# Performance work log

Measured on AMD Instinct MI355X. Metric: run time of the kernel, lower is better.

The kernel has to match this reference:

```python
import jax, jax.numpy as jnp
import numpy as np

B, L, K = 8, 512, 30
H, NUM_IN, NPTS = 128, 384, 8
EPS = 1e-8


def _linear_params(key, din, dout):
    kw, kb = jax.random.split(key)
    W = jax.random.normal(kw, (din, dout), jnp.float32) * 0.02
    b = jax.random.normal(kb, (dout,), jnp.float32) * 0.02
    return W, b


def setup_inputs() -> dict:
    key = jax.random.key(0)
    ks = jax.random.split(key, 10)
    h_V = jax.random.normal(ks[0], (B, L, H), jnp.float32)
    h_E = jax.random.normal(ks[1], (B, L, K, NUM_IN), jnp.float32)
    E_idx = jax.random.randint(ks[2], (B, L, K), 0, L)
    X_neighbors = jax.random.normal(ks[3], (B, L, K, 3, 3), jnp.float32) * 3.0
    mask_V = jnp.ones((B, L), jnp.float32)
    mask_attend = jnp.ones((B, L, K), jnp.float32)
    Wp, bp = _linear_params(ks[4], H, NPTS * 3)
    W1, b1 = _linear_params(ks[5], H + NUM_IN + 9 * NPTS, H)
    W2, b2 = _linear_params(ks[6], H, H)
    W3, b3 = _linear_params(ks[7], H, H)
    Wi, bi = _linear_params(ks[8], H, 4 * H)
    Wo, bo = _linear_params(ks[9], 4 * H, H)
    g1 = jnp.ones((H,), jnp.float32); be1 = jnp.zeros((H,), jnp.float32)
    g2 = jnp.ones((H,), jnp.float32); be2 = jnp.zeros((H,), jnp.float32)
    return dict(h_V=h_V, h_E=h_E, E_idx=E_idx, X_neighbors=X_neighbors,
                mask_V=mask_V, mask_attend=mask_attend,
                Wp=Wp, bp=bp, W1=W1, b1=b1, W2=W2, b2=b2, W3=W3, b3=b3,
                Wi=Wi, bi=bi, Wo=Wo, bo=bo, g1=g1, be1=be1, g2=g2, be2=be2)


def _frames(N, CA, C):
    # openfold Rigid.from_3_points (Gram-Schmidt): x-axis along CA-N, C in xy-plane
    e0 = CA - N
    e0 = e0 / jnp.sqrt(jnp.sum(e0 * e0, -1, keepdims=True) + EPS)
    e1 = C - CA
    e1 = e1 - e0 * jnp.sum(e0 * e1, -1, keepdims=True)
    e1 = e1 / jnp.sqrt(jnp.sum(e1 * e1, -1, keepdims=True) + EPS)
    e2 = jnp.cross(e0, e1)
    R = jnp.stack([e0, e1, e2], axis=-1)  # basis vectors as columns
    return R, CA


def _ln(x, g, b):
    m = jnp.mean(x, -1, keepdims=True)
    v = jnp.var(x, -1, keepdims=True)
    return (x - m) / jnp.sqrt(v + 1e-5) * g + b


def _forward(h_V, h_E, X_neighbors, mask_V, mask_attend, Wp, bp, W1, b1, W2, b2,
             W3, b3, Wi, bi, Wo, bo, g1, be1, g2, be2):
    gelu = lambda x: jax.nn.gelu(x, approximate=False)
    # per-neighbor backbone frames: [B,L,K,3,3], [B,L,K,3]
    R, t = _frames(X_neighbors[..., 0, :], X_neighbors[..., 1, :], X_neighbors[..., 2, :])
    h_V_prev = h_E[..., -H:]
    sh = h_E.shape[:-1]  # (B,L,K)
    p_ln = (h_V_prev @ Wp + bp).reshape(*sh, NPTS, 3)  # local points of each neighbor
    p_local = p_ln[:, :, 0]                            # [B,L,n,3] (self is neighbor 0)
    npg = jnp.einsum('blkij,blknj->blkni', R, p_ln) + t[..., None, :]  # global points
    p_global = npg[:, :, 0]
    pge = jnp.broadcast_to(p_global[:, :, None], npg.shape)
    ple = jnp.broadcast_to(p_local[:, :, None], npg.shape)
    pln = jnp.sqrt(jnp.sum(ple * ple, -1) + EPS)
    R0 = R[:, :, 0]; t0 = t[:, :, 0]  # self frame
    npl = jnp.einsum('blji,blknj->blkni', R0, npg - t0[:, :, None, None, :])  # invert_apply
    npl_norm = jnp.sqrt(jnp.sum(npl * npl, -1) + EPS)
    npg_norm = jnp.sqrt(jnp.sum((pge - npg) ** 2, -1) + EPS)
    node_expand = jnp.broadcast_to(h_V[:, :, None, :], (*sh, H))
    msg = jnp.concatenate([node_expand, h_E,
                           ple.reshape(*sh, -1), pln,
                           npl.reshape(*sh, -1), npl_norm, npg_norm], axis=-1)
    node_m = gelu(msg @ W1 + b1)
    node_m = gelu(node_m @ W2 + b2)
    node_m = node_m @ W3 + b3
    node_m = mask_attend[..., None] * node_m
    node_m = jnp.mean(node_m, axis=-2)
    h = _ln(h_V + node_m, g1, be1)  # dropout is identity in eval
    d = gelu(h @ Wi + bi) @ Wo + bo
    h = _ln(h + d, g2, be2)
    return mask_V[..., None] * h


def reference(h_V, h_E, E_idx, X_neighbors, mask_V, mask_attend, Wp, bp, W1, b1,
              W2, b2, W3, b3, Wi, bi, Wo, bo, g1, be1, g2, be2):
    # E_idx only defines the neighbor axis shape; geometry comes pre-gathered in X_neighbors/h_E
    return _forward(h_V, h_E, X_neighbors, mask_V, mask_attend, Wp, bp, W1, b1,
                    W2, b2, W3, b3, Wi, bi, Wo, bo, g1, be1, g2, be2)
```

## Files before the change

kernel.cpp:

```cpp
#include <hip/hip_runtime.h>

#define B_ 8
#define L_ 512
#define K_ 30
#define NIN_ 384
#define HES 11520
#define BUFW 136
#define GFW 96
#define PWU 4608
#define R0_OFF 0
#define T0_OFF 9
#define PL0_OFF 12
#define NPG_OFF 40
#define PLF_OFF 760
#define NM_OFF 640
#define GEOF_OFF 1520

#define W1F_OFF 0
#define W2F_OFF 77824
#define W3F_OFF 94208
#define WIF_OFF 110592
#define WOF_OFF 176128
#define WPF_OFF 241664

typedef __attribute__((ext_vector_type(8))) short short8;
typedef __attribute__((ext_vector_type(8))) unsigned short ushort8;
typedef __attribute__((ext_vector_type(4))) float floatx4;
typedef __attribute__((ext_vector_type(4))) float f32x4;

__device__ __forceinline__ float b2f(unsigned short u) {
    union { unsigned int i; float f; } x; x.i = ((unsigned int)u) << 16; return x.f;
}
__device__ __forceinline__ unsigned short f2b(float f) {
    unsigned int u = __builtin_bit_cast(unsigned int, f);
    return (unsigned short)((u + 0x7fffu + ((u >> 16) & 1u)) >> 16);
}
__device__ __forceinline__ float gelu_f(float x) {
    return 0.5f * x * (1.0f + erff(x * 0.70710678118654752440f));
}
__device__ __forceinline__ short8 pack8(const float* p) {
    f32x4 lo = *(const f32x4*)p;
    f32x4 hi = *(const f32x4*)(p + 4);
    short8 r;
    r[0] = (short)f2b(lo[0]); r[1] = (short)f2b(lo[1]);
    r[2] = (short)f2b(lo[2]); r[3] = (short)f2b(lo[3]);
    r[4] = (short)f2b(hi[0]); r[5] = (short)f2b(hi[1]);
    r[6] = (short)f2b(hi[2]); r[7] = (short)f2b(hi[3]);
    return r;
}
__device__ __forceinline__ float dot8(const float* hp, ushort8 v) {
    return hp[0] * b2f(v[0]) + hp[1] * b2f(v[1]) + hp[2] * b2f(v[2]) + hp[3] * b2f(v[3]) +
           hp[4] * b2f(v[4]) + hp[5] * b2f(v[5]) + hp[6] * b2f(v[6]) + hp[7] * b2f(v[7]);
}

__global__ __launch_bounds__(256) void prep_kernel(
        const float* __restrict__ W1, const float* __restrict__ W2,
        const float* __restrict__ W3, const float* __restrict__ Wi,
        const float* __restrict__ Wo, const float* __restrict__ Wp,
        unsigned short* __restrict__ ws) {
    int idx = blockIdx.x * 256 + threadIdx.x;
    if (idx < 94208 || (idx >= 241664 && idx < 245760)) {
        const float* in; int i, KC, Kreal, Nreal, Nld;
        if (idx < 77824)      { in = W1; i = idx;          KC = 19; Kreal = 584; Nreal = 128; Nld = 128; }
        else if (idx < 94208) { in = W2; i = idx - 77824;  KC = 4;  Kreal = 128; Nreal = 128; Nld = 128; }
        else                  { in = Wp; i = idx - 241664; KC = 4;  Kreal = 128; Nreal = 24;  Nld = 24;  }
        int f = i >> 9, r = i & 511;
        int ct = f / KC, kc = f % KC;
        int lane = r >> 3, j = r & 7;
        int q = lane >> 4, l = lane & 15;
        int k = kc * 32 + q * 8 + j, n = ct * 16 + l;
        ws[idx] = (k < Kreal && n < Nreal) ? f2b(in[k * Nld + n]) : (unsigned short)0;
    } else if (idx < 110592) {
        int i = idx - 94208;
        int f = i >> 9, r = i & 511;
        int ct = f >> 2, kc = f & 3;
        int lane = r >> 3, j = r & 7;
        int q = lane >> 4, l = lane & 15;
        ws[idx] = f2b(W3[(kc * 32 + q * 8 + j) * 128 + ct * 16 + l]);
    } else if (idx < 176128) {
        int i = idx - 110592;
        int c8 = i >> 12, r = i & 4095;
        int o = r >> 3, ii = r & 7;
        ws[idx] = f2b(Wi[(c8 * 8 + ii) * 512 + o]);
    } else if (idx < 241664) {
        int i = idx - 176128;
        int o8 = i >> 10, r = i & 1023;
        int c = r >> 3, ii = r & 7;
        ws[idx] = f2b(Wo[(o8 * 8 + ii) * 128 + c]);
    }
}

__global__ __launch_bounds__(128, 3) void main_kernel(
    const float* __restrict__ h_V,
    const float* __restrict__ h_E,
    const float* __restrict__ Xn,
    const float* __restrict__ mask_V,
    const float* __restrict__ mask_attend,
    const float* __restrict__ bp,
    const float* __restrict__ b1g,
    const float* __restrict__ b2g,
    const float* __restrict__ b3g,
    const float* __restrict__ big,
    const float* __restrict__ bog,
    const float* __restrict__ g1,
    const float* __restrict__ be1,
    const float* __restrict__ g2,
    const float* __restrict__ be2,
    const unsigned short* __restrict__ wsT,
    float* __restrict__ out) {

    __shared__ __align__(16) unsigned short lds[2 * PWU];

    const int tid  = threadIdx.x;
    const int wv   = tid >> 6;
    const int lane = tid & 63;
    const int quad = lane >> 4;
    const int l16  = lane & 15;
    const int ko   = quad * 8;
    const int site = blockIdx.x * 2 + wv;

    unsigned short* wl   = lds + wv * PWU;
    unsigned short* buf1 = wl;
    unsigned short* geoF = wl + GEOF_OFF;
    float*          Fv   = (float*)wl;

    const unsigned short* W1F = wsT + W1F_OFF;
    const unsigned short* W2F = wsT + W2F_OFF;
    const unsigned short* W3F = wsT + W3F_OFF;
    const unsigned short* WiF = wsT + WIF_OFF;
    const unsigned short* WoF = wsT + WOF_OFF;
    const unsigned short* WpF = wsT + WPF_OFF;

    const float* hEb = h_E + (size_t)site * HES;
    const float* hVb = h_V + site * 128;
    const short8 z8 = {0, 0, 0, 0, 0, 0, 0, 0};

    float maskR[2][4];
    for (int rt = 0; rt < 2; ++rt)
        for (int r = 0; r < 4; ++r) {
            int row = rt * 16 + quad * 4 + r;
            maskR[rt][r] = (row < K_) ? mask_attend[site * K_ + row] * (1.0f / 30.0f) : 0.0f;
        }

    float Rr[9], Tt[3];
    if (lane < K_) {
        const float* xp = Xn + ((size_t)site * K_ + lane) * 9;
        float Nx = xp[0], Ny = xp[1], Nz = xp[2];
        float Ax = xp[3], Ay = xp[4], Az = xp[5];
        float Cx = xp[6], Cy = xp[7], Cz = xp[8];
        float e0x = Ax - Nx, e0y = Ay - Ny, e0z = Az - Nz;
        float r0 = 1.0f / sqrtf(e0x * e0x + e0y * e0y + e0z * e0z + 1e-8f);
        e0x *= r0; e0y *= r0; e0z *= r0;
        float u1x = Cx - Ax, u1y = Cy - Ay, u1z = Cz - Az;
        float d = e0x * u1x + e0y * u1y + e0z * u1z;
        u1x -= e0x * d; u1y -= e0y * d; u1z -= e0z * d;
        float r1 = 1.0f / sqrtf(u1x * u1x + u1y * u1y + u1z * u1z + 1e-8f);
        u1x *= r1; u1y *= r1; u1z *= r1;
        Rr[0] = e0x; Rr[1] = u1x; Rr[2] = e0y * u1z - e0z * u1y;
        Rr[3] = e0y; Rr[4] = u1y; Rr[5] = e0z * u1x - e0x * u1z;
        Rr[6] = e0z; Rr[7] = u1z; Rr[8] = e0x * u1y - e0y * u1x;
        Tt[0] = Ax; Tt[1] = Ay; Tt[2] = Az;
    }

    {
        floatx4 a[2][2] = {{{0,0,0,0},{0,0,0,0}},{{0,0,0,0},{0,0,0,0}}};
        for (int kc = 0; kc < 4; ++kc) {
            int col = 256 + kc * 32 + ko;
            short8 fa0 = pack8(hEb + l16 * NIN_ + col);
            int r1 = 16 + l16;
            short8 fa1 = (r1 < K_) ? pack8(hEb + r1 * NIN_ + col) : z8;
            for (int ct = 0; ct < 2; ++ct) {
                short8 fb = *(const short8*)(WpF + (ct * 4 + kc) * 512 + lane * 8);
                a[0][ct] = __builtin_amdgcn_mfma_f32_16x16x32_bf16(fa0, fb, a[0][ct], 0, 0, 0);
                a[1][ct] = __builtin_amdgcn_mfma_f32_16x16x32_bf16(fa1, fb, a[1][ct], 0, 0, 0);
            }
        }
        for (int ct = 0; ct < 2; ++ct) {
            int ccol = ct * 16 + l16;
            if (ccol < 24) {
                float bpc = bp[ccol];
                for (int rt = 0; rt < 2; ++rt)
                    for (int i = 0; i < 4; ++i) {
                        int row = rt * 16 + quad * 4 + i;
                        if (row < K_) Fv[PLF_OFF + row * 24 + ccol] = a[rt][ct][i] + bpc;
                    }
            }
        }
    }

    if (lane < K_) {
        float pl[24];
        #pragma unroll
        for (int c = 0; c < 24; ++c) pl[c] = Fv[PLF_OFF + lane * 24 + c];
        if (lane == 0) {
            #pragma unroll
            for (int i = 0; i < 9; ++i) Fv[R0_OFF + i] = Rr[i];
            Fv[T0_OFF] = Tt[0]; Fv[T0_OFF + 1] = Tt[1]; Fv[T0_OFF + 2] = Tt[2];
            #pragma unroll
            for (int c = 0; c < 24; ++c) Fv[PL0_OFF + c] = pl[c];
        }
        #pragma unroll
        for (int n = 0; n < 8; ++n) {
            float p0 = pl[n * 3], p1 = pl[n * 3 + 1], p2 = pl[n * 3 + 2];
            #pragma unroll
            for (int i = 0; i < 3; ++i)
                Fv[NPG_OFF + lane * 24 + n * 3 + i] =
                    Rr[i * 3 + 0] * p0 + Rr[i * 3 + 1] * p1 + Rr[i * 3 + 2] * p2 + Tt[i];
        }
    }

    for (int id = lane; id < 720; id += 64) geoF[(id / 24) * GFW + 72 + id % 24] = 0;
    {
        float R00 = Fv[0], R01 = Fv[1], R02 = Fv[2], R03 = Fv[3], R04 = Fv[4];
        float R05 = Fv[5], R06 = Fv[6], R07 = Fv[7], R08 = Fv[8];
        float T00 = Fv[9], T01 = Fv[10], T02 = Fv[11];
        for (int id = lane; id < 240; id += 64) {
            int k = id >> 3, n = id & 7;
            float p0 = Fv[PL0_OFF + n * 3], p1 = Fv[PL0_OFF + n * 3 + 1], p2 = Fv[PL0_OFF + n * 3 + 2];
            float q0g = Fv[NPG_OFF + n * 3], q1g = Fv[NPG_OFF + n * 3 + 1], q2g = Fv[NPG_OFF + n * 3 + 2];
            float a0 = Fv[NPG_OFF + k * 24 + n * 3];
            float a1 = Fv[NPG_OFF + k * 24 + n * 3 + 1];
            float a2 = Fv[NPG_OFF + k * 24 + n * 3 + 2];
            float d0 = a0 - T00, d1 = a1 - T01, d2 = a2 - T02;
            float nl0 = R00 * d0 + R03 * d1 + R06 * d2;
            float nl1 = R01 * d0 + R04 * d1 + R07 * d2;
            float nl2 = R02 * d0 + R05 * d1 + R08 * d2;
            unsigned short* gf = geoF + k * GFW;
            gf[0 + n * 3] = f2b(p0); gf[1 + n * 3] = f2b(p1); gf[2 + n * 3] = f2b(p2);
            gf[24 + n] = f2b(sqrtf(p0 * p0 + p1 * p1 + p2 * p2 + 1e-8f));
            gf[32 + n * 3] = f2b(nl0); gf[33 + n * 3] = f2b(nl1); gf[34 + n * 3] = f2b(nl2);
            gf[56 + n] = f2b(sqrtf(nl0 * nl0 + nl1 * nl1 + nl2 * nl2 + 1e-8f));
            float q0 = q0g - a0, q1 = q1g - a1, q2 = q2g - a2;
            gf[64 + n] = f2b(sqrtf(q0 * q0 + q1 * q1 + q2 * q2 + 1e-8f));
        }
    }

    {
        floatx4 acc[2][8];
        for (int rt = 0; rt < 2; ++rt) for (int ct = 0; ct < 8; ++ct) acc[rt][ct] = (floatx4){0,0,0,0};
        for (int kc = 0; kc < 4; ++kc) {
            int col = kc * 32 + ko;
            short8 fa = pack8(hVb + col);
            for (int ct = 0; ct < 8; ++ct) {
                short8 fb = *(const short8*)(W1F + (ct * 19 + kc) * 512 + lane * 8);
                acc[0][ct] = __builtin_amdgcn_mfma_f32_16x16x32_bf16(fa, fb, acc[0][ct], 0, 0, 0);
                acc[1][ct] = __builtin_amdgcn_mfma_f32_16x16x32_bf16(fa, fb, acc[1][ct], 0, 0, 0);
            }
        }
        for (int kc = 0; kc < 12; ++kc) {
            int col = kc * 32 + ko;
            short8 fa0 = pack8(hEb + l16 * NIN_ + col);
            int r1 = 16 + l16;
            short8 fa1 = (r1 < K_) ? pack8(hEb + r1 * NIN_ + col) : z8;
            for (int ct = 0; ct < 8; ++ct) {
                short8 fb = *(const short8*)(W1F + (ct * 19 + 4 + kc) * 512 + lane * 8);
                acc[0][ct] = __builtin_amdgcn_mfma_f32_16x16x32_bf16(fa0, fb, acc[0][ct], 0, 0, 0);
                acc[1][ct] = __builtin_amdgcn_mfma_f32_16x16x32_bf16(fa1, fb, acc[1][ct], 0, 0, 0);
            }
        }
        for (int kc = 0; kc < 3; ++kc) {
            int col = kc * 32 + ko;
            short8 fa0 = *(const short8*)&geoF[l16 * GFW + col];
            int r1 = 16 + l16;
            short8 fa1 = (r1 < K_) ? *(const short8*)&geoF[r1 * GFW + col] : z8;
            for (int ct = 0; ct < 8; ++ct) {
                short8 fb = *(const short8*)(W1F + (ct * 19 + 16 + kc) * 512 + lane * 8);
                acc[0][ct] = __builtin_amdgcn_mfma_f32_16x16x32_bf16(fa0, fb, acc[0][ct], 0, 0, 0);
                acc[1][ct] = __builtin_amdgcn_mfma_f32_16x16x32_bf16(fa1, fb, acc[1][ct], 0, 0, 0);
            }
        }
        for (int ct = 0; ct < 8; ++ct) {
            int col = ct * 16 + l16;
            float bb = b1g[col];
            for (int rt = 0; rt < 2; ++rt)
                for (int r = 0; r < 4; ++r) {
                    int row = rt * 16 + quad * 4 + r;
                    buf1[row * BUFW + col] = f2b(gelu_f(acc[rt][ct][r] + bb));
                }
        }
    }

    {
        short8 Af[2][4];
        for (int kc = 0; kc < 4; ++kc) {
            Af[0][kc] = *(const short8*)&buf1[l16 * BUFW + kc * 32 + ko];
            Af[1][kc] = *(const short8*)&buf1[(16 + l16) * BUFW + kc * 32 + ko];
        }
        floatx4 acc[2][8];
        for (int rt = 0; rt < 2; ++rt) for (int ct = 0; ct < 8; ++ct) acc[rt][ct] = (floatx4){0,0,0,0};
        for (int kc = 0; kc < 4; ++kc)
            for (int ct = 0; ct < 8; ++ct) {
                short8 fb = *(const short8*)(W2F + (ct * 4 + kc) * 512 + lane * 8);
                acc[0][ct] = __builtin_amdgcn_mfma_f32_16x16x32_bf16(Af[0][kc], fb, acc[0][ct], 0, 0, 0);
                acc[1][ct] = __builtin_amdgcn_mfma_f32_16x16x32_bf16(Af[1][kc], fb, acc[1][ct], 0, 0, 0);
            }
        for (int ct = 0; ct < 8; ++ct) {
            int col = ct * 16 + l16;
            float bb = b2g[col];
            for (int rt = 0; rt < 2; ++rt)
                for (int r = 0; r < 4; ++r) {
                    int row = rt * 16 + quad * 4 + r;
                    buf1[row * BUFW + col] = f2b(gelu_f(acc[rt][ct][r] + bb));
                }
        }
    }

    {
        short8 Af[2][4];
        for (int kc = 0; kc < 4; ++kc) {
            Af[0][kc] = *(const short8*)&buf1[l16 * BUFW + kc * 32 + ko];
            Af[1][kc] = *(const short8*)&buf1[(16 + l16) * BUFW + kc * 32 + ko];
        }
        floatx4 acc[2][8];
        for (int rt = 0; rt < 2; ++rt) for (int ct = 0; ct < 8; ++ct) acc[rt][ct] = (floatx4){0,0,0,0};
        for (int kc = 0; kc < 4; ++kc)
            for (int ct = 0; ct < 8; ++ct) {
                short8 fb = *(const short8*)(W3F + (ct * 4 + kc) * 512 + lane * 8);
                acc[0][ct] = __builtin_amdgcn_mfma_f32_16x16x32_bf16(Af[0][kc], fb, acc[0][ct], 0, 0, 0);
                acc[1][ct] = __builtin_amdgcn_mfma_f32_16x16x32_bf16(Af[1][kc], fb, acc[1][ct], 0, 0, 0);
            }
        for (int ct = 0; ct < 8; ++ct) {
            int col = ct * 16 + l16;
            float bb = b3g[col];
            float cs = 0.0f;
            for (int rt = 0; rt < 2; ++rt)
                for (int r = 0; r < 4; ++r)
                    cs += (acc[rt][ct][r] + bb) * maskR[rt][r];
            cs += __shfl_xor(cs, 16, 64);
            cs += __shfl_xor(cs, 32, 64);
            if (lane < 16) Fv[NM_OFF + col] = cs;
        }
    }

    {
        int c0 = lane, c1 = lane + 64;
        float xb0 = hVb[c0] + Fv[NM_OFF + c0];
        float xb1 = hVb[c1] + Fv[NM_OFF + c1];
        float s = xb0 + xb1, q = xb0 * xb0 + xb1 * xb1;
        for (int o = 32; o; o >>= 1) { s += __shfl_xor(s, o, 64); q += __shfl_xor(q, o, 64); }
        float m = s * (1.0f / 128.0f);
        float inv = 1.0f / sqrtf(q * (1.0f / 128.0f) - m * m + 1e-5f);
        float h0 = (xb0 - m) * inv * g1[c0] + be1[c0];
        float h1 = (xb1 - m) * inv * g1[c1] + be1[c1];
        Fv[c0] = h0; Fv[c1] = h1;

        for (int j = 0; j < 8; ++j) {
            int o = lane + 64 * j;
            float sa = big[o], sb = 0.0f;
            for (int c8 = 0; c8 < 16; c8 += 2) {
                ushort8 v0 = *(const ushort8*)(WiF + c8 * 4096 + o * 8);
                ushort8 v1 = *(const ushort8*)(WiF + (c8 + 1) * 4096 + o * 8);
                sa += dot8(&Fv[c8 * 8], v0);
                sb += dot8(&Fv[c8 * 8 + 8], v1);
            }
            Fv[128 + o] = gelu_f(sa + sb);
        }

        float d0a = bog[c0], d0b = 0.0f, d1a = bog[c1], d1b = 0.0f;
        for (int o8 = 0; o8 < 64; o8 += 2) {
            ushort8 v0  = *(const ushort8*)(WoF + o8 * 1024 + c0 * 8);
            ushort8 v0n = *(const ushort8*)(WoF + (o8 + 1) * 1024 + c0 * 8);
            ushort8 v1  = *(const ushort8*)(WoF + o8 * 1024 + c1 * 8);
            ushort8 v1n = *(const ushort8*)(WoF + (o8 + 1) * 1024 + c1 * 8);
            const float* gp = &Fv[128 + o8 * 8];
            d0a += dot8(gp, v0);  d0b += dot8(gp + 8, v0n);
            d1a += dot8(gp, v1);  d1b += dot8(gp + 8, v1n);
        }
        float y0 = h0 + d0a + d0b, y1 = h1 + d1a + d1b;
        float s2 = y0 + y1, q2 = y0 * y0 + y1 * y1;
        for (int o = 32; o; o >>= 1) { s2 += __shfl_xor(s2, o, 64); q2 += __shfl_xor(q2, o, 64); }
        float m2 = s2 * (1.0f / 128.0f);
        float inv2 = 1.0f / sqrtf(q2 * (1.0f / 128.0f) - m2 * m2 + 1e-5f);
        float mv = mask_V[site];
        out[site * 128 + c0] = ((y0 - m2) * inv2 * g2[c0] + be2[c0]) * mv;
        out[site * 128 + c1] = ((y1 - m2) * inv2 * g2[c1] + be2[c1]) * mv;
    }
}

extern "C" void kernel_launch(void* const* d_in, const int* in_sizes, int n_in,
                              void* d_out, int out_size, void* d_ws, size_t ws_size,
                              hipStream_t stream) {
    const float* h_V = (const float*)d_in[0];
    const float* h_E = (const float*)d_in[1];
    const float* Xn  = (const float*)d_in[3];
    const float* mV  = (const float*)d_in[4];
    const float* mA  = (const float*)d_in[5];
    const float* Wp  = (const float*)d_in[6];
    const float* bp  = (const float*)d_in[7];
    const float* W1  = (const float*)d_in[8];
    const float* b1  = (const float*)d_in[9];
    const float* W2  = (const float*)d_in[10];
    const float* b2  = (const float*)d_in[11];
    const float* W3  = (const float*)d_in[12];
    const float* b3  = (const float*)d_in[13];
    const float* Wi  = (const float*)d_in[14];
    const float* bi  = (const float*)d_in[15];
    const float* Wo  = (const float*)d_in[16];
    const float* bo  = (const float*)d_in[17];
    const float* g1  = (const float*)d_in[18];
    const float* be1 = (const float*)d_in[19];
    const float* g2  = (const float*)d_in[20];
    const float* be2 = (const float*)d_in[21];
    unsigned short* ws = (unsigned short*)d_ws;
    float* out = (float*)d_out;

    prep_kernel<<<960, 256, 0, stream>>>(W1, W2, W3, Wi, Wo, Wp, ws);
    main_kernel<<<(B_ * L_) / 2, 128, 0, stream>>>(h_V, h_E, Xn, mV, mA, bp,
                                                   b1, b2, b3, bi, bo,
                                                   g1, be1, g2, be2, ws, out);
}
```

Before: 444.6 us.

## Pre-cast h_E and h_V to bf16 in a separate pass, use one-wave blocks

Adds a cast kernel that converts h_E and h_V to bf16 in workspace memory. The main kernel then loads bf16 fragments directly instead of reading fp32 and packing to bf16 on every pass over h_E. The main kernel also changes from two-wave blocks to single-wave blocks, one site per block. The cast adds a full extra read and write pass over the largest input. The new path only runs when the workspace is large enough; otherwise it falls back to the fp32 loads.

```diff
diff --git a/kernel.cpp b/kernel.cpp
--- a/kernel.cpp
+++ b/kernel.cpp
@@ -22,6 +22,9 @@
 #define WIF_OFF 110592
 #define WOF_OFF 176128
 #define WPF_OFF 241664
+#define HE16_OFF 245760ULL
+#define HV16_OFF (245760ULL + 47185920ULL)
+#define NEED_BYTES ((HV16_OFF + 524288ULL) * 2ULL)
 
 typedef __attribute__((ext_vector_type(8))) short short8;
 typedef __attribute__((ext_vector_type(8))) unsigned short ushort8;
@@ -90,7 +93,27 @@
     }
 }
 
-__global__ __launch_bounds__(128, 3) void main_kernel(
+__global__ __launch_bounds__(256) void cast_kernel(
+        const float* __restrict__ h_E, const float* __restrict__ h_V,
+        unsigned short* __restrict__ ws) {
+    const long long NHE8 = 47185920LL / 8;
+    const long long NTOT = NHE8 + 524288LL / 8;
+    long long stride = (long long)gridDim.x * 256;
+    for (long long i = (long long)blockIdx.x * 256 + threadIdx.x; i < NTOT; i += stride) {
+        const float* src; unsigned short* dst;
+        if (i < NHE8) { src = h_E + i * 8;            dst = ws + HE16_OFF + i * 8; }
+        else          { long long j = i - NHE8; src = h_V + j * 8; dst = ws + HV16_OFF + j * 8; }
+        f32x4 lo = *(const f32x4*)src;
+        f32x4 hi = *(const f32x4*)(src + 4);
+        ushort8 o;
+        o[0] = f2b(lo[0]); o[1] = f2b(lo[1]); o[2] = f2b(lo[2]); o[3] = f2b(lo[3]);
+        o[4] = f2b(hi[0]); o[5] = f2b(hi[1]); o[6] = f2b(hi[2]); o[7] = f2b(hi[3]);
+        *(ushort8*)dst = o;
+    }
+}
+
+template <int USEB>
+__global__ __launch_bounds__(64, 3) void main_kernel(
     const float* __restrict__ h_V,
     const float* __restrict__ h_E,
     const float* __restrict__ Xn,
@@ -109,17 +132,14 @@
     const unsigned short* __restrict__ wsT,
     float* __restrict__ out) {
 
-    __shared__ __align__(16) unsigned short lds[2 * PWU];
-
-    const int tid  = threadIdx.x;
-    const int wv   = tid >> 6;
-    const int lane = tid & 63;
+    __shared__ __align__(16) unsigned short wl[PWU];
+
+    const int lane = threadIdx.x;
     const int quad = lane >> 4;
     const int l16  = lane & 15;
     const int ko   = quad * 8;
-    const int site = blockIdx.x * 2 + wv;
-
-    unsigned short* wl   = lds + wv * PWU;
+    const int site = blockIdx.x;
+
     unsigned short* buf1 = wl;
     unsigned short* geoF = wl + GEOF_OFF;
     float*          Fv   = (float*)wl;
@@ -133,6 +153,8 @@
 
     const float* hEb = h_E + (size_t)site * HES;
     const float* hVb = h_V + site * 128;
+    const unsigned short* hE16 = wsT + HE16_OFF + (size_t)site * HES;
+    const unsigned short* hV16 = wsT + HV16_OFF + (size_t)site * 128;
     const short8 z8 = {0, 0, 0, 0, 0, 0, 0, 0};
 
     float maskR[2][4];
@@ -166,9 +188,15 @@
         floatx4 a[2][2] = {{{0,0,0,0},{0,0,0,0}},{{0,0,0,0},{0,0,0,0}}};
         for (int kc = 0; kc < 4; ++kc) {
             int col = 256 + kc * 32 + ko;
-            short8 fa0 = pack8(hEb + l16 * NIN_ + col);
+            short8 fa0, fa1;
             int r1 = 16 + l16;
-            short8 fa1 = (r1 < K_) ? pack8(hEb + r1 * NIN_ + col) : z8;
+            if (USEB) {
+                fa0 = *(const short8*)(hE16 + l16 * NIN_ + col);
+                fa1 = (r1 < K_) ? *(const short8*)(hE16 + r1 * NIN_ + col) : z8;
+            } else {
+                fa0 = pack8(hEb + l16 * NIN_ + col);
+                fa1 = (r1 < K_) ? pack8(hEb + r1 * NIN_ + col) : z8;
+            }
             for (int ct = 0; ct < 2; ++ct) {
                 short8 fb = *(const short8*)(WpF + (ct * 4 + kc) * 512 + lane * 8);
                 a[0][ct] = __builtin_amdgcn_mfma_f32_16x16x32_bf16(fa0, fb, a[0][ct], 0, 0, 0);
@@ -240,7 +268,7 @@
         for (int rt = 0; rt < 2; ++rt) for (int ct = 0; ct < 8; ++ct) acc[rt][ct] = (floatx4){0,0,0,0};
         for (int kc = 0; kc < 4; ++kc) {
             int col = kc * 32 + ko;
-            short8 fa = pack8(hVb + col);
+            short8 fa = USEB ? *(const short8*)(hV16 + col) : pack8(hVb + col);
             for (int ct = 0; ct < 8; ++ct) {
                 short8 fb = *(const short8*)(W1F + (ct * 19 + kc) * 512 + lane * 8);
                 acc[0][ct] = __builtin_amdgcn_mfma_f32_16x16x32_bf16(fa, fb, acc[0][ct], 0, 0, 0);
@@ -249,9 +277,15 @@
         }
         for (int kc = 0; kc < 12; ++kc) {
             int col = kc * 32 + ko;
-            short8 fa0 = pack8(hEb + l16 * NIN_ + col);
+            short8 fa0, fa1;
             int r1 = 16 + l16;
-            short8 fa1 = (r1 < K_) ? pack8(hEb + r1 * NIN_ + col) : z8;
+            if (USEB) {
+                fa0 = *(const short8*)(hE16 + l16 * NIN_ + col);
+                fa1 = (r1 < K_) ? *(const short8*)(hE16 + r1 * NIN_ + col) : z8;
+            } else {
+                fa0 = pack8(hEb + l16 * NIN_ + col);
+                fa1 = (r1 < K_) ? pack8(hEb + r1 * NIN_ + col) : z8;
+            }
             for (int ct = 0; ct < 8; ++ct) {
                 short8 fb = *(const short8*)(W1F + (ct * 19 + 4 + kc) * 512 + lane * 8);
                 acc[0][ct] = __builtin_amdgcn_mfma_f32_16x16x32_bf16(fa0, fb, acc[0][ct], 0, 0, 0);
@@ -405,7 +439,14 @@
     float* out = (float*)d_out;
 
     prep_kernel<<<960, 256, 0, stream>>>(W1, W2, W3, Wi, Wo, Wp, ws);
-    main_kernel<<<(B_ * L_) / 2, 128, 0, stream>>>(h_V, h_E, Xn, mV, mA, bp,
+    if (ws_size >= (size_t)NEED_BYTES) {
+        cast_kernel<<<2048, 256, 0, stream>>>(h_E, h_V, ws);
+        main_kernel<1><<<B_ * L_, 64, 0, stream>>>(h_V, h_E, Xn, mV, mA, bp,
                                                    b1, b2, b3, bi, bo,
                                                    g1, be1, g2, be2, ws, out);
-}
+    } else {
+        main_kernel<0><<<B_ * L_, 64, 0, stream>>>(h_V, h_E, Xn, mV, mA, bp,
+                                                   b1, b2, b3, bi, bo,
+                                                   g1, be1, g2, be2, ws, out);
+    }
+}
```

Result: slower. 605.9 us (+36.3%).
